# Optimization experiments

Hardware: AMD Instinct MI355X
Metric: run time of the kernel (lower is better)

## Reference

```python
import jax, jax.numpy as jnp
import numpy as np

B, S, E, H = 2, 512, 1024, 16
D = E // H  # 64


def setup_inputs() -> dict:
    key = jax.random.key(0)
    ks = jax.random.split(key, 8)
    q = jax.random.normal(ks[0], (B, S, E), dtype=jnp.float32)
    k = jax.random.normal(ks[1], (B, S, E), dtype=jnp.float32)
    v = jax.random.normal(ks[2], (B, S, E), dtype=jnp.float32)
    # per-position bilinear term, scaled down so scores stay in a sane range
    p = jax.random.normal(ks[3], (B, S, H, D, D), dtype=jnp.float32) * 0.05
    # causal additive mask [S, S]
    neg = jnp.float32(-1e9)
    mask = jnp.where(jnp.triu(jnp.ones((S, S), dtype=bool), k=1), neg, jnp.float32(0.0))
    scale = 1.0 / np.sqrt(E)
    Wq = jax.random.normal(ks[4], (E, E), dtype=jnp.float32) * scale
    Wk = jax.random.normal(ks[5], (E, E), dtype=jnp.float32) * scale
    Wv = jax.random.normal(ks[6], (E, E), dtype=jnp.float32) * scale
    Wo = jax.random.normal(ks[7], (E, E), dtype=jnp.float32) * scale
    return {"q": q, "k": k, "v": v, "p": p, "mask": mask,
            "Wq": Wq, "Wk": Wk, "Wv": Wv, "Wo": Wo}


def reference(q, k, v, p, mask, Wq, Wk, Wv, Wo):
    b, s, e = q.shape
    h, d = p.shape[2], p.shape[3]
    # projections (torch Linear: y = x @ W.T), split into heads -> [b,h,s,d]
    qh = (q @ Wq.T).reshape(b, s, h, d).transpose(0, 2, 1, 3)
    kh = (k @ Wk.T).reshape(b, -1, h, d).transpose(0, 2, 1, 3)
    vh = (v @ Wv.T).reshape(b, -1, h, d).transpose(0, 2, 1, 3)
    # scores = einsum('bhse,bshef,bhtf->bhst') done in two steps
    qp = jnp.einsum('bhse,bshef->bhsf', qh, p)          # [b,h,s,d]
    scores = jnp.einsum('bhsf,bhtf->bhst', qp, kh)      # [b,h,s,t]
    scores = scores / jnp.sqrt(jnp.float32(d))
    scores = scores + mask[None, None, :, :]
    w = jax.nn.softmax(scores, axis=-1)
    att = jnp.einsum('bhst,bhtd->bshd', w, vh).reshape(b, s, e)
    return att @ Wo.T
```

## Files before the change

kernel.cpp:

```cpp
#include <hip/hip_runtime.h>
#include <hip/hip_bf16.h>

namespace {

constexpr int kB = 2, kS = 512, kE = 1024, kH = 16, kD = 64;
constexpr int kM = kB * kS;
constexpr int kBH = kB * kH;
constexpr int kSP = 524;

typedef short bf16x8 __attribute__((ext_vector_type(8)));
typedef float f32x4 __attribute__((ext_vector_type(4)));

__device__ __forceinline__ unsigned short f2bf(float f) {
  __hip_bfloat16 h = __float2bfloat16(f);
  unsigned short u;
  __builtin_memcpy(&u, &h, 2);
  return u;
}
__device__ __forceinline__ float bf2f(unsigned short u) {
  unsigned int x = (unsigned int)u << 16;
  float f;
  __builtin_memcpy(&f, &x, 4);
  return f;
}

__global__ void cvt7_kernel(const float* __restrict__ s0, const float* __restrict__ s1,
                            const float* __restrict__ s2, const float* __restrict__ s3,
                            const float* __restrict__ s4, const float* __restrict__ s5,
                            const float* __restrict__ s6,
                            unsigned short* __restrict__ dstBase) {
  const float* srcs[7] = {s0, s1, s2, s3, s4, s5, s6};
  const float* src = srcs[blockIdx.y];
  unsigned short* dst = dstBase + (size_t)blockIdx.y * (kM * kE);
  int i = (blockIdx.x * blockDim.x + threadIdx.x) * 4;
  float4 v = *reinterpret_cast<const float4*>(src + i);
  ushort4 o;
  o.x = f2bf(v.x); o.y = f2bf(v.y); o.z = f2bf(v.z); o.w = f2bf(v.w);
  *reinterpret_cast<ushort4*>(dst + i) = o;
}

__device__ __forceinline__ void mfma_tile_32x32(
    const unsigned short* __restrict__ A, int lda,
    const unsigned short* __restrict__ Bm, int ldb,
    int row0, int col0, int K, f32x4 acc[2][2]) {
  const int lane = threadIdx.x & 63;
  const int r = lane & 15;
  const int ko = (lane >> 4) * 8;
  const unsigned short* a0 = A + (size_t)(row0 + r) * lda + ko;
  const unsigned short* a1 = a0 + 16 * (size_t)lda;
  const unsigned short* b0 = Bm + (size_t)(col0 + r) * ldb + ko;
  const unsigned short* b1 = b0 + 16 * (size_t)ldb;
  for (int kk = 0; kk < K; kk += 32) {
    bf16x8 af0 = *reinterpret_cast<const bf16x8*>(a0 + kk);
    bf16x8 af1 = *reinterpret_cast<const bf16x8*>(a1 + kk);
    bf16x8 bg0 = *reinterpret_cast<const bf16x8*>(b0 + kk);
    bf16x8 bg1 = *reinterpret_cast<const bf16x8*>(b1 + kk);
    acc[0][0] = __builtin_amdgcn_mfma_f32_16x16x32_bf16(af0, bg0, acc[0][0], 0, 0, 0);
    acc[0][1] = __builtin_amdgcn_mfma_f32_16x16x32_bf16(af0, bg1, acc[0][1], 0, 0, 0);
    acc[1][0] = __builtin_amdgcn_mfma_f32_16x16x32_bf16(af1, bg0, acc[1][0], 0, 0, 0);
    acc[1][1] = __builtin_amdgcn_mfma_f32_16x16x32_bf16(af1, bg1, acc[1][1], 0, 0, 0);
  }
}

__global__ __launch_bounds__(256) void proj_q_kernel(
    const unsigned short* __restrict__ qb, const unsigned short* __restrict__ Wq,
    unsigned short* __restrict__ qh) {
  const int w = threadIdx.x >> 6;
  const int row0 = blockIdx.y * 64 + (w >> 1) * 32;
  const int col0 = blockIdx.x * 64 + (w & 1) * 32;
  f32x4 acc[2][2] = {};
  mfma_tile_32x32(qb, kE, Wq, kE, row0, col0, kE, acc);
  const int lane = threadIdx.x & 63;
#pragma unroll
  for (int ri = 0; ri < 2; ++ri)
#pragma unroll
    for (int ci = 0; ci < 2; ++ci)
#pragma unroll
      for (int r = 0; r < 4; ++r) {
        int i = row0 + 16 * ri + 4 * (lane >> 4) + r;
        int j = col0 + 16 * ci + (lane & 15);
        int b = i >> 9, s = i & 511, h = j >> 6, d = j & 63;
        qh[(((size_t)(b * kH + h) * kS) + s) * kD + d] = f2bf(acc[ri][ci][r]);
      }
}

__global__ __launch_bounds__(256) void mega_kernel(
    const float* __restrict__ p, const unsigned short* __restrict__ qh,
    unsigned short* __restrict__ qp,
    const unsigned short* __restrict__ kb, const unsigned short* __restrict__ vb,
    const unsigned short* __restrict__ Wk, const unsigned short* __restrict__ Wv,
    unsigned short* __restrict__ kh, unsigned short* __restrict__ vhT) {
  __shared__ float qsh[kH][kD];
  const int flat = blockIdx.x;
  const int mod = flat % 3;
  if (mod == 2) {
    const int pidx = flat / 3;
    const int which = pidx >> 8;
    const int tile = pidx & 255;
    const int w = threadIdx.x >> 6;
    const int row0 = (tile >> 4) * 64 + (w >> 1) * 32;
    const int col0 = (tile & 15) * 64 + (w & 1) * 32;
    const unsigned short* A = which ? vb : kb;
    const unsigned short* W = which ? Wv : Wk;
    f32x4 acc[2][2] = {};
    mfma_tile_32x32(A, kE, W, kE, row0, col0, kE, acc);
    const int lane = threadIdx.x & 63;
#pragma unroll
    for (int ri = 0; ri < 2; ++ri)
#pragma unroll
      for (int ci = 0; ci < 2; ++ci)
#pragma unroll
        for (int r = 0; r < 4; ++r) {
          int i = row0 + 16 * ri + 4 * (lane >> 4) + r;
          int j = col0 + 16 * ci + (lane & 15);
          int b = i >> 9, s = i & 511, h = j >> 6, d = j & 63;
          unsigned short val = f2bf(acc[ri][ci][r]);
          if (which)
            vhT[(((size_t)(b * kH + h) * kD) + d) * kS + s] = val;
          else
            kh[(((size_t)(b * kH + h) * kS) + s) * kD + d] = val;
        }
  } else {
    const int bs = (flat / 3) * 2 + mod;
    const int b = bs >> 9, s = bs & 511;
    const int t = threadIdx.x;
    {
      int h = t >> 4, d4 = (t & 15) * 4;
      const unsigned short* qr =
          qh + (((size_t)(b * kH + h) * kS) + s) * kD + d4;
      ushort4 u = *reinterpret_cast<const ushort4*>(qr);
      qsh[h][d4 + 0] = bf2f(u.x);
      qsh[h][d4 + 1] = bf2f(u.y);
      qsh[h][d4 + 2] = bf2f(u.z);
      qsh[h][d4 + 3] = bf2f(u.w);
    }
    __syncthreads();
    const int h = t >> 4, fi = t & 15;
    const float4* p4 =
        reinterpret_cast<const float4*>(p + ((size_t)(bs * kH + h) << 12));
    float4 acc = {0.f, 0.f, 0.f, 0.f};
#pragma unroll 4
    for (int e = 0; e < kD; ++e) {
      float4 pv = p4[e * 16 + fi];
      float qv = qsh[h][e];
      acc.x += qv * pv.x;
      acc.y += qv * pv.y;
      acc.z += qv * pv.z;
      acc.w += qv * pv.w;
    }
    ushort4 o;
    o.x = f2bf(acc.x); o.y = f2bf(acc.y); o.z = f2bf(acc.z); o.w = f2bf(acc.w);
    *reinterpret_cast<ushort4*>(
        qp + (((size_t)(b * kH + h) * kS) + s) * kD + fi * 4) = o;
  }
}

__global__ __launch_bounds__(256) void attn_kernel(
    const unsigned short* __restrict__ qp,
    const unsigned short* __restrict__ kh,
    const unsigned short* __restrict__ vhT,
    unsigned short* __restrict__ att) {
  __shared__ float S[32 * kSP];
  const int bh = blockIdx.y;
  const int b = bh >> 4, h = bh & 15;
  const int bx = blockIdx.x;
  const int row0 = bx * 32;
  const int ncol = row0 + 32;
  const int w = threadIdx.x >> 6;
  const int lane = threadIdx.x & 63;
  const int g = lane >> 4, c = lane & 15;

  const unsigned short* Abase = qp + (size_t)bh * kS * kD;
  const unsigned short* Kbase = kh + (size_t)bh * kS * kD;

  bf16x8 qa[2][2];
#pragma unroll
  for (int ri = 0; ri < 2; ++ri)
#pragma unroll
    for (int kk = 0; kk < 2; ++kk)
      qa[ri][kk] = *reinterpret_cast<const bf16x8*>(
          Abase + (size_t)(row0 + 16 * ri + c) * kD + kk * 32 + g * 8);

  for (int ct = w; ct <= bx; ct += 4) {
    const int col0 = ct * 32;
    const unsigned short* kr0 = Kbase + (size_t)(col0 + c) * kD + g * 8;
    bf16x8 kb00 = *reinterpret_cast<const bf16x8*>(kr0);
    bf16x8 kb01 = *reinterpret_cast<const bf16x8*>(kr0 + 32);
    bf16x8 kb10 = *reinterpret_cast<const bf16x8*>(kr0 + 16 * kD);
    bf16x8 kb11 = *reinterpret_cast<const bf16x8*>(kr0 + 16 * kD + 32);
    f32x4 sacc[2][2] = {};
    sacc[0][0] = __builtin_amdgcn_mfma_f32_16x16x32_bf16(qa[0][0], kb00, sacc[0][0], 0, 0, 0);
    sacc[0][0] = __builtin_amdgcn_mfma_f32_16x16x32_bf16(qa[0][1], kb01, sacc[0][0], 0, 0, 0);
    sacc[0][1] = __builtin_amdgcn_mfma_f32_16x16x32_bf16(qa[0][0], kb10, sacc[0][1], 0, 0, 0);
    sacc[0][1] = __builtin_amdgcn_mfma_f32_16x16x32_bf16(qa[0][1], kb11, sacc[0][1], 0, 0, 0);
    sacc[1][0] = __builtin_amdgcn_mfma_f32_16x16x32_bf16(qa[1][0], kb00, sacc[1][0], 0, 0, 0);
    sacc[1][0] = __builtin_amdgcn_mfma_f32_16x16x32_bf16(qa[1][1], kb01, sacc[1][0], 0, 0, 0);
    sacc[1][1] = __builtin_amdgcn_mfma_f32_16x16x32_bf16(qa[1][0], kb10, sacc[1][1], 0, 0, 0);
    sacc[1][1] = __builtin_amdgcn_mfma_f32_16x16x32_bf16(qa[1][1], kb11, sacc[1][1], 0, 0, 0);
#pragma unroll
    for (int ri = 0; ri < 2; ++ri)
#pragma unroll
      for (int ci = 0; ci < 2; ++ci)
#pragma unroll
        for (int r = 0; r < 4; ++r) {
          int il = 16 * ri + 4 * g + r;
          int jg = col0 + 16 * ci + c;
          float val = sacc[ri][ci][r] * 0.125f;
          if (jg > row0 + il) val = -1e9f;
          S[il * kSP + jg] = val;
        }
  }
  __syncthreads();

#pragma unroll
  for (int rr = 0; rr < 8; ++rr) {
    const int i = w * 8 + rr;
    float v[8];
    float m = -1e30f;
#pragma unroll
    for (int ii = 0; ii < 8; ++ii) {
      int j = lane + 64 * ii;
      v[ii] = (j < ncol) ? S[i * kSP + j] : -1e30f;
      m = fmaxf(m, v[ii]);
    }
#pragma unroll
    for (int off = 32; off; off >>= 1) m = fmaxf(m, __shfl_xor(m, off));
    float e[8], sum = 0.f;
#pragma unroll
    for (int ii = 0; ii < 8; ++ii) {
      e[ii] = __expf(v[ii] - m);
      sum += e[ii];
    }
#pragma unroll
    for (int off = 32; off; off >>= 1) sum += __shfl_xor(sum, off);
    const float inv = 1.0f / sum;
#pragma unroll
    for (int ii = 0; ii < 8; ++ii) S[i * kSP + lane + 64 * ii] = e[ii] * inv;
  }
  __syncthreads();

  const int d0 = w * 16;
  const unsigned short* Vbase = vhT + (size_t)(bh * kD + d0 + c) * kS;
  f32x4 oacc[2] = {};
  const int nk = bx + 1;
  for (int ks = 0; ks < nk; ++ks) {
    const int kb = ks * 32;
    bf16x8 vfrag = *reinterpret_cast<const bf16x8*>(Vbase + kb + g * 8);
#pragma unroll
    for (int ri = 0; ri < 2; ++ri) {
      const float* sp = &S[(16 * ri + c) * kSP + kb + g * 8];
      float4 x0 = *reinterpret_cast<const float4*>(sp);
      float4 x1 = *reinterpret_cast<const float4*>(sp + 4);
      bf16x8 pa;
      pa[0] = (short)f2bf(x0.x); pa[1] = (short)f2bf(x0.y);
      pa[2] = (short)f2bf(x0.z); pa[3] = (short)f2bf(x0.w);
      pa[4] = (short)f2bf(x1.x); pa[5] = (short)f2bf(x1.y);
      pa[6] = (short)f2bf(x1.z); pa[7] = (short)f2bf(x1.w);
      oacc[ri] = __builtin_amdgcn_mfma_f32_16x16x32_bf16(pa, vfrag, oacc[ri], 0, 0, 0);
    }
  }
#pragma unroll
  for (int ri = 0; ri < 2; ++ri)
#pragma unroll
    for (int r = 0; r < 4; ++r) {
      int s = row0 + 16 * ri + 4 * g + r;
      int d = d0 + c;
      att[((size_t)(b * kS + s) * kE) + h * kD + d] = f2bf(oacc[ri][r]);
    }
}

__global__ __launch_bounds__(256) void out_kernel(
    const unsigned short* __restrict__ att, const unsigned short* __restrict__ Wo,
    float* __restrict__ out) {
  const int w = threadIdx.x >> 6;
  const int row0 = blockIdx.y * 64 + (w >> 1) * 32;
  const int col0 = blockIdx.x * 64 + (w & 1) * 32;
  f32x4 acc[2][2] = {};
  mfma_tile_32x32(att, kE, Wo, kE, row0, col0, kE, acc);
  const int lane = threadIdx.x & 63;
#pragma unroll
  for (int ri = 0; ri < 2; ++ri)
#pragma unroll
    for (int ci = 0; ci < 2; ++ci)
#pragma unroll
      for (int r = 0; r < 4; ++r) {
        int i = row0 + 16 * ri + 4 * (lane >> 4) + r;
        int j = col0 + 16 * ci + (lane & 15);
        out[(size_t)i * kE + j] = acc[ri][ci][r];
      }
}

}

extern "C" void kernel_launch(void* const* d_in, const int* in_sizes, int n_in,
                              void* d_out, int out_size, void* d_ws,
                              size_t ws_size, hipStream_t stream) {
  const float* q = (const float*)d_in[0];
  const float* k = (const float*)d_in[1];
  const float* v = (const float*)d_in[2];
  const float* p = (const float*)d_in[3];
  const float* Wq = (const float*)d_in[5];
  const float* Wk = (const float*)d_in[6];
  const float* Wv = (const float*)d_in[7];
  const float* Wo = (const float*)d_in[8];
  float* out = (float*)d_out;

  char* ws = (char*)d_ws;
  size_t off = 0;
  auto alloc = [&](size_t bytes) {
    void* ptr = ws + off;
    off += (bytes + 255) & ~(size_t)255;
    return ptr;
  };
  const size_t nME = (size_t)kM * kE;
  unsigned short* qb = (unsigned short*)alloc(nME * 2);
  unsigned short* kb = (unsigned short*)alloc(nME * 2);
  unsigned short* vb = (unsigned short*)alloc(nME * 2);
  unsigned short* Wqb = (unsigned short*)alloc(nME * 2);
  unsigned short* Wkb = (unsigned short*)alloc(nME * 2);
  unsigned short* Wvb = (unsigned short*)alloc(nME * 2);
  unsigned short* Wob = (unsigned short*)alloc(nME * 2);
  unsigned short* qhB = (unsigned short*)alloc(nME * 2);
  unsigned short* khB = (unsigned short*)alloc(nME * 2);
  unsigned short* vhTB = (unsigned short*)alloc(nME * 2);
  unsigned short* qpB = (unsigned short*)alloc(nME * 2);
  unsigned short* attB = (unsigned short*)alloc(nME * 2);

  cvt7_kernel<<<dim3(kM * kE / (256 * 4), 7), 256, 0, stream>>>(
      q, k, v, Wq, Wk, Wv, Wo, qb);

  proj_q_kernel<<<dim3(kE / 64, kM / 64), 256, 0, stream>>>(qb, Wqb, qhB);

  mega_kernel<<<1536, 256, 0, stream>>>(p, qhB, qpB, kb, vb, Wkb, Wvb, khB,
                                        vhTB);

  attn_kernel<<<dim3(kS / 32, kBH), 256, 0, stream>>>(qpB, khB, vhTB, attB);

  out_kernel<<<dim3(kE / 64, kM / 64), 256, 0, stream>>>(attB, Wob, out);
}
```

Measured before the change: 144.6 us.

## Split qp contraction across wave lanes with shuffle reduction, more blocks

Each wave now computes qp for one (b,s,h) tuple. The four 16-lane groups each reduce over 16 of the 64 e values, and the partial sums are combined with cross-lane shuffles, so the shared-memory staging and the block barrier are gone. The grid grows from 1536 to 4608 blocks, which keeps a 1:8 interleave between projection tiles and qp blocks. The aim is more parallelism and shorter per-thread dependency chains on the memory-bound streaming of p, at the cost of shuffle work and only a quarter of the lanes doing the final store.

```diff
diff --git a/kernel.cpp b/kernel.cpp
--- a/kernel.cpp
+++ b/kernel.cpp
@@ -10,6 +10,7 @@
 
 typedef short bf16x8 __attribute__((ext_vector_type(8)));
 typedef float f32x4 __attribute__((ext_vector_type(4)));
+typedef unsigned short u16x8 __attribute__((ext_vector_type(8)));
 
 __device__ __forceinline__ unsigned short f2bf(float f) {
   __hip_bfloat16 h = __float2bfloat16(f);
@@ -90,11 +91,10 @@
     const unsigned short* __restrict__ kb, const unsigned short* __restrict__ vb,
     const unsigned short* __restrict__ Wk, const unsigned short* __restrict__ Wv,
     unsigned short* __restrict__ kh, unsigned short* __restrict__ vhT) {
-  __shared__ float qsh[kH][kD];
   const int flat = blockIdx.x;
-  const int mod = flat % 3;
-  if (mod == 2) {
-    const int pidx = flat / 3;
+  const int r9 = flat % 9;
+  if (r9 == 4) {
+    const int pidx = flat / 9;
     const int which = pidx >> 8;
     const int tile = pidx & 255;
     const int w = threadIdx.x >> 6;
@@ -121,37 +121,51 @@
             kh[(((size_t)(b * kH + h) * kS) + s) * kD + d] = val;
         }
   } else {
-    const int bs = (flat / 3) * 2 + mod;
-    const int b = bs >> 9, s = bs & 511;
-    const int t = threadIdx.x;
+    const int qpblk = flat - flat / 9 - (r9 > 4 ? 1 : 0);
+    const int w = threadIdx.x >> 6;
+    const int lane = threadIdx.x & 63;
+    const int tid = qpblk * 4 + w;
+    const int g = lane >> 4, fi = lane & 15;
+    const int bs = tid >> 4;
+    const int b = bs >> 9, s = bs & 511, h = tid & 15;
+
+    const unsigned short* qrow =
+        qh + (((size_t)(b * kH + h) * kS) + s) * kD + 16 * g;
+    float qv[16];
     {
-      int h = t >> 4, d4 = (t & 15) * 4;
-      const unsigned short* qr =
-          qh + (((size_t)(b * kH + h) * kS) + s) * kD + d4;
-      ushort4 u = *reinterpret_cast<const ushort4*>(qr);
-      qsh[h][d4 + 0] = bf2f(u.x);
-      qsh[h][d4 + 1] = bf2f(u.y);
-      qsh[h][d4 + 2] = bf2f(u.z);
-      qsh[h][d4 + 3] = bf2f(u.w);
-    }
-    __syncthreads();
-    const int h = t >> 4, fi = t & 15;
-    const float4* p4 =
-        reinterpret_cast<const float4*>(p + ((size_t)(bs * kH + h) << 12));
+      u16x8 u0 = *reinterpret_cast<const u16x8*>(qrow);
+      u16x8 u1 = *reinterpret_cast<const u16x8*>(qrow + 8);
+#pragma unroll
+      for (int i = 0; i < 8; ++i) {
+        qv[i] = bf2f(u0[i]);
+        qv[8 + i] = bf2f(u1[i]);
+      }
+    }
+    const float4* p4 = reinterpret_cast<const float4*>(p) +
+                       (size_t)tid * 1024 + g * 256 + fi;
     float4 acc = {0.f, 0.f, 0.f, 0.f};
-#pragma unroll 4
-    for (int e = 0; e < kD; ++e) {
-      float4 pv = p4[e * 16 + fi];
-      float qv = qsh[h][e];
-      acc.x += qv * pv.x;
-      acc.y += qv * pv.y;
-      acc.z += qv * pv.z;
-      acc.w += qv * pv.w;
-    }
-    ushort4 o;
-    o.x = f2bf(acc.x); o.y = f2bf(acc.y); o.z = f2bf(acc.z); o.w = f2bf(acc.w);
-    *reinterpret_cast<ushort4*>(
-        qp + (((size_t)(b * kH + h) * kS) + s) * kD + fi * 4) = o;
+#pragma unroll
+    for (int ei = 0; ei < 16; ++ei) {
+      float4 pv = p4[ei * 16];
+      acc.x += qv[ei] * pv.x;
+      acc.y += qv[ei] * pv.y;
+      acc.z += qv[ei] * pv.z;
+      acc.w += qv[ei] * pv.w;
+    }
+    acc.x += __shfl_xor(acc.x, 16);
+    acc.y += __shfl_xor(acc.y, 16);
+    acc.z += __shfl_xor(acc.z, 16);
+    acc.w += __shfl_xor(acc.w, 16);
+    acc.x += __shfl_xor(acc.x, 32);
+    acc.y += __shfl_xor(acc.y, 32);
+    acc.z += __shfl_xor(acc.z, 32);
+    acc.w += __shfl_xor(acc.w, 32);
+    if (g == 0) {
+      ushort4 o;
+      o.x = f2bf(acc.x); o.y = f2bf(acc.y); o.z = f2bf(acc.z); o.w = f2bf(acc.w);
+      *reinterpret_cast<ushort4*>(
+          qp + (((size_t)(b * kH + h) * kS) + s) * kD + fi * 4) = o;
+    }
   }
 }
 
@@ -331,7 +345,7 @@
 
   proj_q_kernel<<<dim3(kE / 64, kM / 64), 256, 0, stream>>>(qb, Wqb, qhB);
 
-  mega_kernel<<<1536, 256, 0, stream>>>(p, qhB, qpB, kb, vb, Wkb, Wvb, khB,
+  mega_kernel<<<4608, 256, 0, stream>>>(p, qhB, qpB, kb, vb, Wkb, Wvb, khB,
                                         vhTB);
 
   attn_kernel<<<dim3(kS / 32, kBH), 256, 0, stream>>>(qpB, khB, vhTB, attB);
```

Result: slower. 151.3 us (+4.7%).

## Fuse fp32-to-bf16 conversion into GEMM operand loads and drop cvt kernel

Applied to the files above, without the earlier changes.

Removes the separate kernel that converted q, k, v and the four weight matrices to bf16. The three projection GEMMs and the output GEMM now read fp32 directly and convert each fragment in registers before the MFMA. This saves one launch and a full write/read pass of 7 bf16 matrices, but every GEMM now loads twice as many bytes per operand from global memory with no shared-memory reuse, and the conversion is repeated for each tile that reads the same data. The p tensor is also read with nontemporal loads, since it is streamed only once.

```diff
diff --git a/kernel.cpp b/kernel.cpp
--- a/kernel.cpp
+++ b/kernel.cpp
@@ -10,6 +10,7 @@
 
 typedef short bf16x8 __attribute__((ext_vector_type(8)));
 typedef float f32x4 __attribute__((ext_vector_type(4)));
+typedef unsigned short u16x8 __attribute__((ext_vector_type(8)));
 
 __device__ __forceinline__ unsigned short f2bf(float f) {
   __hip_bfloat16 h = __float2bfloat16(f);
@@ -24,37 +25,33 @@
   return f;
 }
 
-__global__ void cvt7_kernel(const float* __restrict__ s0, const float* __restrict__ s1,
-                            const float* __restrict__ s2, const float* __restrict__ s3,
-                            const float* __restrict__ s4, const float* __restrict__ s5,
-                            const float* __restrict__ s6,
-                            unsigned short* __restrict__ dstBase) {
-  const float* srcs[7] = {s0, s1, s2, s3, s4, s5, s6};
-  const float* src = srcs[blockIdx.y];
-  unsigned short* dst = dstBase + (size_t)blockIdx.y * (kM * kE);
-  int i = (blockIdx.x * blockDim.x + threadIdx.x) * 4;
-  float4 v = *reinterpret_cast<const float4*>(src + i);
-  ushort4 o;
-  o.x = f2bf(v.x); o.y = f2bf(v.y); o.z = f2bf(v.z); o.w = f2bf(v.w);
-  *reinterpret_cast<ushort4*>(dst + i) = o;
-}
-
-__device__ __forceinline__ void mfma_tile_32x32(
-    const unsigned short* __restrict__ A, int lda,
-    const unsigned short* __restrict__ Bm, int ldb,
-    int row0, int col0, int K, f32x4 acc[2][2]) {
+__device__ __forceinline__ bf16x8 f32frag(const float* __restrict__ ptr) {
+  f32x4 a = *reinterpret_cast<const f32x4*>(ptr);
+  f32x4 b = *reinterpret_cast<const f32x4*>(ptr + 4);
+  bf16x8 r;
+#pragma unroll
+  for (int i = 0; i < 4; ++i) {
+    r[i] = (short)f2bf(a[i]);
+    r[4 + i] = (short)f2bf(b[i]);
+  }
+  return r;
+}
+
+__device__ __forceinline__ void mfma_tile_32x32_f32(
+    const float* __restrict__ A, int lda, const float* __restrict__ Bm,
+    int ldb, int row0, int col0, int K, f32x4 acc[2][2]) {
   const int lane = threadIdx.x & 63;
   const int r = lane & 15;
   const int ko = (lane >> 4) * 8;
-  const unsigned short* a0 = A + (size_t)(row0 + r) * lda + ko;
-  const unsigned short* a1 = a0 + 16 * (size_t)lda;
-  const unsigned short* b0 = Bm + (size_t)(col0 + r) * ldb + ko;
-  const unsigned short* b1 = b0 + 16 * (size_t)ldb;
+  const float* a0 = A + (size_t)(row0 + r) * lda + ko;
+  const float* a1 = a0 + 16 * (size_t)lda;
+  const float* b0 = Bm + (size_t)(col0 + r) * ldb + ko;
+  const float* b1 = b0 + 16 * (size_t)ldb;
   for (int kk = 0; kk < K; kk += 32) {
-    bf16x8 af0 = *reinterpret_cast<const bf16x8*>(a0 + kk);
-    bf16x8 af1 = *reinterpret_cast<const bf16x8*>(a1 + kk);
-    bf16x8 bg0 = *reinterpret_cast<const bf16x8*>(b0 + kk);
-    bf16x8 bg1 = *reinterpret_cast<const bf16x8*>(b1 + kk);
+    bf16x8 af0 = f32frag(a0 + kk);
+    bf16x8 af1 = f32frag(a1 + kk);
+    bf16x8 bg0 = f32frag(b0 + kk);
+    bf16x8 bg1 = f32frag(b1 + kk);
     acc[0][0] = __builtin_amdgcn_mfma_f32_16x16x32_bf16(af0, bg0, acc[0][0], 0, 0, 0);
     acc[0][1] = __builtin_amdgcn_mfma_f32_16x16x32_bf16(af0, bg1, acc[0][1], 0, 0, 0);
     acc[1][0] = __builtin_amdgcn_mfma_f32_16x16x32_bf16(af1, bg0, acc[1][0], 0, 0, 0);
@@ -63,13 +60,13 @@
 }
 
 __global__ __launch_bounds__(256) void proj_q_kernel(
-    const unsigned short* __restrict__ qb, const unsigned short* __restrict__ Wq,
+    const float* __restrict__ q, const float* __restrict__ Wq,
     unsigned short* __restrict__ qh) {
   const int w = threadIdx.x >> 6;
   const int row0 = blockIdx.y * 64 + (w >> 1) * 32;
   const int col0 = blockIdx.x * 64 + (w & 1) * 32;
   f32x4 acc[2][2] = {};
-  mfma_tile_32x32(qb, kE, Wq, kE, row0, col0, kE, acc);
+  mfma_tile_32x32_f32(q, kE, Wq, kE, row0, col0, kE, acc);
   const int lane = threadIdx.x & 63;
 #pragma unroll
   for (int ri = 0; ri < 2; ++ri)
@@ -87,8 +84,8 @@
 __global__ __launch_bounds__(256) void mega_kernel(
     const float* __restrict__ p, const unsigned short* __restrict__ qh,
     unsigned short* __restrict__ qp,
-    const unsigned short* __restrict__ kb, const unsigned short* __restrict__ vb,
-    const unsigned short* __restrict__ Wk, const unsigned short* __restrict__ Wv,
+    const float* __restrict__ kin, const float* __restrict__ vin,
+    const float* __restrict__ Wk, const float* __restrict__ Wv,
     unsigned short* __restrict__ kh, unsigned short* __restrict__ vhT) {
   __shared__ float qsh[kH][kD];
   const int flat = blockIdx.x;
@@ -100,10 +97,10 @@
     const int w = threadIdx.x >> 6;
     const int row0 = (tile >> 4) * 64 + (w >> 1) * 32;
     const int col0 = (tile & 15) * 64 + (w & 1) * 32;
-    const unsigned short* A = which ? vb : kb;
-    const unsigned short* W = which ? Wv : Wk;
+    const float* A = which ? vin : kin;
+    const float* W = which ? Wv : Wk;
     f32x4 acc[2][2] = {};
-    mfma_tile_32x32(A, kE, W, kE, row0, col0, kE, acc);
+    mfma_tile_32x32_f32(A, kE, W, kE, row0, col0, kE, acc);
     const int lane = threadIdx.x & 63;
 #pragma unroll
     for (int ri = 0; ri < 2; ++ri)
@@ -136,20 +133,20 @@
     }
     __syncthreads();
     const int h = t >> 4, fi = t & 15;
-    const float4* p4 =
-        reinterpret_cast<const float4*>(p + ((size_t)(bs * kH + h) << 12));
-    float4 acc = {0.f, 0.f, 0.f, 0.f};
+    const f32x4* p4 =
+        reinterpret_cast<const f32x4*>(p + ((size_t)(bs * kH + h) << 12));
+    f32x4 acc = {0.f, 0.f, 0.f, 0.f};
 #pragma unroll 4
     for (int e = 0; e < kD; ++e) {
-      float4 pv = p4[e * 16 + fi];
+      f32x4 pv = __builtin_nontemporal_load(p4 + e * 16 + fi);
       float qv = qsh[h][e];
-      acc.x += qv * pv.x;
-      acc.y += qv * pv.y;
-      acc.z += qv * pv.z;
-      acc.w += qv * pv.w;
+      acc[0] += qv * pv[0];
+      acc[1] += qv * pv[1];
+      acc[2] += qv * pv[2];
+      acc[3] += qv * pv[3];
     }
     ushort4 o;
-    o.x = f2bf(acc.x); o.y = f2bf(acc.y); o.z = f2bf(acc.z); o.w = f2bf(acc.w);
+    o.x = f2bf(acc[0]); o.y = f2bf(acc[1]); o.z = f2bf(acc[2]); o.w = f2bf(acc[3]);
     *reinterpret_cast<ushort4*>(
         qp + (((size_t)(b * kH + h) * kS) + s) * kD + fi * 4) = o;
   }
@@ -270,23 +267,38 @@
 }
 
 __global__ __launch_bounds__(256) void out_kernel(
-    const unsigned short* __restrict__ att, const unsigned short* __restrict__ Wo,
+    const unsigned short* __restrict__ att, const float* __restrict__ Wo,
     float* __restrict__ out) {
   const int w = threadIdx.x >> 6;
   const int row0 = blockIdx.y * 64 + (w >> 1) * 32;
   const int col0 = blockIdx.x * 64 + (w & 1) * 32;
+  const int lane = threadIdx.x & 63;
+  const int r = lane & 15;
+  const int ko = (lane >> 4) * 8;
+  const unsigned short* a0 = att + (size_t)(row0 + r) * kE + ko;
+  const unsigned short* a1 = a0 + 16 * (size_t)kE;
+  const float* b0 = Wo + (size_t)(col0 + r) * kE + ko;
+  const float* b1 = b0 + 16 * (size_t)kE;
   f32x4 acc[2][2] = {};
-  mfma_tile_32x32(att, kE, Wo, kE, row0, col0, kE, acc);
-  const int lane = threadIdx.x & 63;
+  for (int kk = 0; kk < kE; kk += 32) {
+    bf16x8 af0 = *reinterpret_cast<const bf16x8*>(a0 + kk);
+    bf16x8 af1 = *reinterpret_cast<const bf16x8*>(a1 + kk);
+    bf16x8 bg0 = f32frag(b0 + kk);
+    bf16x8 bg1 = f32frag(b1 + kk);
+    acc[0][0] = __builtin_amdgcn_mfma_f32_16x16x32_bf16(af0, bg0, acc[0][0], 0, 0, 0);
+    acc[0][1] = __builtin_amdgcn_mfma_f32_16x16x32_bf16(af0, bg1, acc[0][1], 0, 0, 0);
+    acc[1][0] = __builtin_amdgcn_mfma_f32_16x16x32_bf16(af1, bg0, acc[1][0], 0, 0, 0);
+    acc[1][1] = __builtin_amdgcn_mfma_f32_16x16x32_bf16(af1, bg1, acc[1][1], 0, 0, 0);
+  }
 #pragma unroll
   for (int ri = 0; ri < 2; ++ri)
 #pragma unroll
     for (int ci = 0; ci < 2; ++ci)
 #pragma unroll
-      for (int r = 0; r < 4; ++r) {
-        int i = row0 + 16 * ri + 4 * (lane >> 4) + r;
+      for (int rr = 0; rr < 4; ++rr) {
+        int i = row0 + 16 * ri + 4 * (lane >> 4) + rr;
         int j = col0 + 16 * ci + (lane & 15);
-        out[(size_t)i * kE + j] = acc[ri][ci][r];
+        out[(size_t)i * kE + j] = acc[ri][ci][rr];
       }
 }
 
@@ -313,28 +325,17 @@
     return ptr;
   };
   const size_t nME = (size_t)kM * kE;
-  unsigned short* qb = (unsigned short*)alloc(nME * 2);
-  unsigned short* kb = (unsigned short*)alloc(nME * 2);
-  unsigned short* vb = (unsigned short*)alloc(nME * 2);
-  unsigned short* Wqb = (unsigned short*)alloc(nME * 2);
-  unsigned short* Wkb = (unsigned short*)alloc(nME * 2);
-  unsigned short* Wvb = (unsigned short*)alloc(nME * 2);
-  unsigned short* Wob = (unsigned short*)alloc(nME * 2);
   unsigned short* qhB = (unsigned short*)alloc(nME * 2);
   unsigned short* khB = (unsigned short*)alloc(nME * 2);
   unsigned short* vhTB = (unsigned short*)alloc(nME * 2);
   unsigned short* qpB = (unsigned short*)alloc(nME * 2);
   unsigned short* attB = (unsigned short*)alloc(nME * 2);
 
-  cvt7_kernel<<<dim3(kM * kE / (256 * 4), 7), 256, 0, stream>>>(
-      q, k, v, Wq, Wk, Wv, Wo, qb);
-
-  proj_q_kernel<<<dim3(kE / 64, kM / 64), 256, 0, stream>>>(qb, Wqb, qhB);
-
-  mega_kernel<<<1536, 256, 0, stream>>>(p, qhB, qpB, kb, vb, Wkb, Wvb, khB,
-                                        vhTB);
+  proj_q_kernel<<<dim3(kE / 64, kM / 64), 256, 0, stream>>>(q, Wq, qhB);
+
+  mega_kernel<<<1536, 256, 0, stream>>>(p, qhB, qpB, k, v, Wk, Wv, khB, vhTB);
 
   attn_kernel<<<dim3(kS / 32, kBH), 256, 0, stream>>>(qpB, khB, vhTB, attB);
 
-  out_kernel<<<dim3(kE / 64, kM / 64), 256, 0, stream>>>(attB, Wob, out);
-}
+  out_kernel<<<dim3(kE / 64, kM / 64), 256, 0, stream>>>(attB, Wo, out);
+}
```

Result: slower. 159.8 us (+10.5%).
